# Kernel tuning notes

Measured on AMD Instinct MI355X. Metric: run time of the kernel, lower is better.

The kernel has to match this reference:

```python
import jax, jax.numpy as jnp
import numpy as np

B, S = 32, 4096          # decode batch, kv cache length
HID, H = 5120, 16        # hidden size, local heads
DN, DR, DV = 128, 64, 128  # qk_nope, qk_rope, v head dims
QL, KL = 1536, 512       # q_lora_rank, kv_lora_rank
BASE = 10000.0
EPS = 1e-6
SCALE = (DN + DR) ** -0.5


def rmsnorm(x, w):
    return x * jax.lax.rsqrt(jnp.mean(x * x, axis=-1, keepdims=True) + EPS) * w


def rope_interleaved(x, pos):
    # non-neox (interleaved pairs) rope, per-row positions pos: [B]
    d = x.shape[-1]
    inv = 1.0 / (BASE ** (jnp.arange(0, d, 2, dtype=jnp.float32) / d))  # [d/2]
    fr = pos.astype(jnp.float32)[:, None] * inv                          # [B, d/2]
    cos, sin = jnp.cos(fr), jnp.sin(fr)
    x1, x2 = x[..., 0::2], x[..., 1::2]
    while cos.ndim < x1.ndim:  # broadcast over head dim if present
        cos, sin = cos[:, None], sin[:, None]
    o1 = x1 * cos - x2 * sin
    o2 = x2 * cos + x1 * sin
    return jnp.stack([o1, o2], axis=-1).reshape(x.shape)


def setup_inputs() -> dict:
    key = jax.random.key(0)
    ks = jax.random.split(key, 9)
    w = 0.02  # weight scale for sane activations
    return {
        "hidden_states": jax.random.normal(ks[0], (B, HID), jnp.float32),
        "positions": jax.random.randint(ks[1], (B,), 0, S, jnp.int32),
        "kv_cache_latent": jax.random.normal(ks[2], (B, S, KL), jnp.float32),
        "kv_cache_rope": jax.random.normal(ks[3], (B, S, DR), jnp.float32),
        "w_qkv_a": jax.random.normal(ks[4], (HID, QL + KL + DR), jnp.float32) * w,
        "q_a_norm_w": jnp.ones((QL,), jnp.float32),
        "w_q_b": jax.random.normal(ks[5], (QL, H * (DN + DR)), jnp.float32) * w,
        "kv_a_norm_w": jnp.ones((KL,), jnp.float32),
        "w_kc": jax.random.normal(ks[6], (H, DN, KL), jnp.float32) * w,
        "w_vc": jax.random.normal(ks[7], (H, KL, DV), jnp.float32) * w,
        "w_o": jax.random.normal(ks[8], (H * DV, HID), jnp.float32) * w,
    }


def reference(hidden_states, positions, kv_cache_latent, kv_cache_rope,
              w_qkv_a, q_a_norm_w, w_q_b, kv_a_norm_w, w_kc, w_vc, w_o):
    # fused qkv_a projection -> q_lora | kv latent | k_pe
    qkv = hidden_states @ w_qkv_a                       # [B, QL+KL+DR]
    q_a, latent, k_pe = jnp.split(qkv, [QL, QL + KL], axis=-1)

    # q path: rmsnorm -> q_b_proj -> per-head split nope/pe
    q = (rmsnorm(q_a, q_a_norm_w) @ w_q_b).reshape(B, H, DN + DR)
    q_nope, q_pe = q[..., :DN], q[..., DN:]
    q_pe = rope_interleaved(q_pe, positions)            # [B, H, DR]

    # kv latent path: rmsnorm latent, rope k_pe, write current token into cache
    latent_n = rmsnorm(latent, kv_a_norm_w)             # [B, KL]
    k_pe = rope_interleaved(k_pe, positions)            # [B, DR]
    cache_l = kv_cache_latent.at[:, -1, :].set(latent_n)  # [B, S, KL]
    cache_r = kv_cache_rope.at[:, -1, :].set(k_pe)        # [B, S, DR]

    # weight absorption: q_nope absorbed through w_kc into latent space
    q_abs = jnp.einsum("bhd,hdc->bhc", q_nope, w_kc)    # [B, H, KL]

    # MQA attention over latent KV (1 kv head shared by all q heads)
    scores = (jnp.einsum("bhc,bsc->bhs", q_abs, cache_l)
              + jnp.einsum("bhr,bsr->bhs", q_pe, cache_r)) * SCALE
    attn = jax.nn.softmax(scores, axis=-1)              # [B, H, S]
    ctx = jnp.einsum("bhs,bsc->bhc", attn, cache_l)     # [B, H, KL]

    # un-absorb values through w_vc, then output projection
    out = jnp.einsum("bhc,hcv->bhv", ctx, w_vc).reshape(B, H * DV)
    return out @ w_o                                    # [B, HID]
```

## Files before the change

kernel.cpp:

```cpp
#include <hip/hip_runtime.h>
#include <stdint.h>

#define B_   32
#define S_   4096
#define HID_ 5120
#define H_   16
#define DN_  128
#define DR_  64
#define DV_  128
#define QL_  1536
#define KL_  512
#define KC_  576
#define NQKV_ 2112
#define NQB_  3072
#define EPS_ 1e-6f
#define SCALE_ 0.07216878364870323f

typedef __attribute__((ext_vector_type(4))) float f32x4;
typedef __attribute__((ext_vector_type(8))) short s16x8;
typedef __attribute__((ext_vector_type(4))) unsigned short u16x4;

__device__ __forceinline__ unsigned short f2bf(float f) {
  union { float f; unsigned u; } v; v.f = f;
  unsigned r = v.u + 0x7fffu + ((v.u >> 16) & 1u);
  return (unsigned short)(r >> 16);
}

__global__ void cvt_bf(const float* __restrict__ X, unsigned short* __restrict__ Y, int n4) {
  int i = blockIdx.x * 256 + threadIdx.x;
  if (i < n4) {
    float4 v = ((const float4*)X)[i];
    u16x4 o; o.x = f2bf(v.x); o.y = f2bf(v.y); o.z = f2bf(v.z); o.w = f2bf(v.w);
    ((u16x4*)Y)[i] = o;
  }
}

template<int K, int TK, int N>
__global__ __launch_bounds__(256) void gemm_bf(const unsigned short* __restrict__ Abf,
                                               const float* __restrict__ W,
                                               float* __restrict__ P) {
  int t = threadIdx.x, wave = t >> 6, lane = t & 63;
  int quad = lane >> 4, lo = lane & 15;
  int n0 = blockIdx.x * 64 + wave * 16;
  int k0 = blockIdx.y * TK;
  f32x4 acc0 = {0.f, 0.f, 0.f, 0.f}, acc1 = {0.f, 0.f, 0.f, 0.f};
  const float* wp = W + (size_t)(k0 + quad * 8) * N + n0 + lo;
  const unsigned short* a0p = Abf + (size_t)lo * K + k0 + quad * 8;
  const unsigned short* a1p = Abf + (size_t)(16 + lo) * K + k0 + quad * 8;
#pragma unroll 2
  for (int kk = 0; kk < TK / 32; ++kk) {
    s16x8 a0 = *(const s16x8*)(a0p + kk * 32);
    s16x8 a1 = *(const s16x8*)(a1p + kk * 32);
    float wv[8];
#pragma unroll
    for (int j = 0; j < 8; ++j) wv[j] = wp[((size_t)kk * 32 + j) * N];
    s16x8 bf;
#pragma unroll
    for (int j = 0; j < 8; ++j) bf[j] = (short)f2bf(wv[j]);
    acc0 = __builtin_amdgcn_mfma_f32_16x16x32_bf16(a0, bf, acc0, 0, 0, 0);
    acc1 = __builtin_amdgcn_mfma_f32_16x16x32_bf16(a1, bf, acc1, 0, 0, 0);
  }
  float* p = P + ((size_t)blockIdx.y * B_) * N + n0 + lo;
#pragma unroll
  for (int reg = 0; reg < 4; ++reg) {
    p[(size_t)(quad * 4 + reg) * N]      = acc0[reg];
    p[(size_t)(16 + quad * 4 + reg) * N] = acc1[reg];
  }
}

__global__ void k2a(const float* __restrict__ P1, const float* __restrict__ qw,
                    const float* __restrict__ kvw, const int* __restrict__ pos,
                    unsigned short* __restrict__ qn_bf, float* __restrict__ latent_n,
                    float* __restrict__ kpe_rot, float* __restrict__ cs_buf) {
  int b = blockIdx.x, t = threadIdx.x;
  __shared__ float row[NQKV_];
  __shared__ float red[256], red2[256];
  float sq = 0.f, sl = 0.f;
  for (int n = t; n < NQKV_; n += 256) {
    float s = 0.f;
#pragma unroll
    for (int ks = 0; ks < 16; ++ks) s += P1[((size_t)ks * B_ + b) * NQKV_ + n];
    row[n] = s;
    if (n < QL_) sq += s * s;
    else if (n < QL_ + KL_) sl += s * s;
  }
  red[t] = sq; red2[t] = sl;
  __syncthreads();
  for (int off = 128; off > 0; off >>= 1) {
    if (t < off) { red[t] += red[t + off]; red2[t] += red2[t + off]; }
    __syncthreads();
  }
  float rq = 1.0f / sqrtf(red[0]  / QL_ + EPS_);
  float rl = 1.0f / sqrtf(red2[0] / KL_ + EPS_);
  for (int n = t; n < QL_; n += 256) qn_bf[(size_t)b * QL_ + n] = f2bf(row[n] * rq * qw[n]);
  for (int n = t; n < KL_; n += 256) latent_n[(size_t)b * KL_ + n] = row[QL_ + n] * rl * kvw[n];
  if (t < 32) {
    double inv = exp(-((double)t / 32.0) * log(10000.0));
    float fr = (float)pos[b] * (float)inv;
    float c = (float)cos((double)fr), s = (float)sin((double)fr);
    cs_buf[(b * 32 + t) * 2] = c; cs_buf[(b * 32 + t) * 2 + 1] = s;
    float x1 = row[QL_ + KL_ + 2 * t], x2 = row[QL_ + KL_ + 2 * t + 1];
    kpe_rot[b * DR_ + 2 * t]     = x1 * c - x2 * s;
    kpe_rot[b * DR_ + 2 * t + 1] = x2 * c + x1 * s;
  }
}

__global__ __launch_bounds__(256) void k2c(const float* __restrict__ P2,
                                           const float* __restrict__ w_kc,
                                           const float* __restrict__ cs_buf,
                                           unsigned short* __restrict__ q_cat) {
  int b = blockIdx.y, t = threadIdx.x, wave = t >> 6, lane = t & 63;
  int h = blockIdx.x * 4 + wave;
  __shared__ float qh[4][192];
  for (int j = lane; j < 192; j += 64) {
    float s = 0.f;
    int col = h * 192 + j;
#pragma unroll
    for (int ks = 0; ks < 12; ++ks) s += P2[((size_t)ks * B_ + b) * NQB_ + col];
    qh[wave][j] = s;
  }
  __syncthreads();
  if (lane < 32) {
    float c = cs_buf[(b * 32 + lane) * 2], s = cs_buf[(b * 32 + lane) * 2 + 1];
    float x1 = qh[wave][DN_ + 2 * lane], x2 = qh[wave][DN_ + 2 * lane + 1];
    qh[wave][DN_ + 2 * lane]     = x1 * c - x2 * s;
    qh[wave][DN_ + 2 * lane + 1] = x2 * c + x1 * s;
  }
  __syncthreads();
  float acc[8];
#pragma unroll
  for (int i = 0; i < 8; ++i) acc[i] = 0.f;
  const float* wk = w_kc + (size_t)h * DN_ * KL_;
#pragma unroll 2
  for (int d = 0; d < DN_; ++d) {
    float qd = qh[wave][d];
#pragma unroll
    for (int i = 0; i < 8; ++i)
      acc[i] = fmaf(qd, wk[(size_t)d * KL_ + lane + 64 * i], acc[i]);
  }
  unsigned short* qc = q_cat + ((size_t)b * H_ + h) * KC_;
#pragma unroll
  for (int i = 0; i < 8; ++i) qc[lane + 64 * i] = f2bf(acc[i] * SCALE_);
  qc[KL_ + lane] = f2bf(qh[wave][DN_ + lane] * SCALE_);
}

#define LP_ 584
#define CHUNK_ 256
#define TR_ 32
#define NTL_ 8

__global__ __launch_bounds__(256, 2) void attn(
    const float* __restrict__ cache_l, const float* __restrict__ cache_r,
    const float* __restrict__ latent_n, const float* __restrict__ kpe_rot,
    const unsigned short* __restrict__ q_cat,
    float* __restrict__ ws_acc, float* __restrict__ ws_ml) {
  int chunk = blockIdx.x, b = blockIdx.y;
  int t = threadIdx.x, wave = t >> 6, lane = t & 63;
  int quad = lane >> 4, lo = lane & 15;

  __shared__ __attribute__((aligned(16))) unsigned short Lt[TR_ * LP_];
  __shared__ __attribute__((aligned(16))) unsigned short pb[4][H_ * TR_];

  s16x8 af[18];
  const unsigned short* qc = q_cat + ((size_t)b * H_ + lo) * KC_;
#pragma unroll
  for (int ks = 0; ks < 18; ++ks) af[ks] = *(const s16x8*)(qc + ks * 32 + quad * 8);

  f32x4 accc[NTL_];
#pragma unroll
  for (int i = 0; i < NTL_; ++i) accc[i] = (f32x4){0.f, 0.f, 0.f, 0.f};
  float m_run[4], l_run[4];
#pragma unroll
  for (int r = 0; r < 4; ++r) { m_run[r] = -3.0e38f; l_run[r] = 0.f; }

  int r8 = t >> 3, u = t & 7;

  float4 v[18];
  auto load_tile = [&](int tile) {
    int s = chunk * CHUNK_ + tile * TR_ + r8;
    const float* rl = cache_l + ((size_t)b * S_ + s) * KL_;
    const float* rr = cache_r + ((size_t)b * S_ + s) * DR_;
    if (s == S_ - 1) { rl = latent_n + (size_t)b * KL_; rr = kpe_rot + (size_t)b * DR_; }
#pragma unroll
    for (int j = 0; j < 18; ++j) {
      int c = u * 4 + j * 32;
      v[j] = *(const float4*)((j < 16) ? (rl + c) : (rr + (c - 512)));
    }
  };
  load_tile(0);

#pragma unroll 1
  for (int tile = 0; tile < NTL_; ++tile) {
    __syncthreads();
#pragma unroll
    for (int j = 0; j < 18; ++j) {
      int c = u * 4 + j * 32;
      u16x4 o; o.x = f2bf(v[j].x); o.y = f2bf(v[j].y); o.z = f2bf(v[j].z); o.w = f2bf(v[j].w);
      *(u16x4*)(&Lt[r8 * LP_ + c]) = o;
    }
    if (tile + 1 < NTL_) load_tile(tile + 1);
    __syncthreads();
    f32x4 sc0 = {0.f, 0.f, 0.f, 0.f}, sc1 = {0.f, 0.f, 0.f, 0.f};
#pragma unroll
    for (int ks = 0; ks < 18; ++ks) {
      s16x8 b0 = *(const s16x8*)(&Lt[lo * LP_ + ks * 32 + quad * 8]);
      s16x8 b1 = *(const s16x8*)(&Lt[(16 + lo) * LP_ + ks * 32 + quad * 8]);
      sc0 = __builtin_amdgcn_mfma_f32_16x16x32_bf16(af[ks], b0, sc0, 0, 0, 0);
      sc1 = __builtin_amdgcn_mfma_f32_16x16x32_bf16(af[ks], b1, sc1, 0, 0, 0);
    }
#pragma unroll
    for (int reg = 0; reg < 4; ++reg) {
      float s0 = sc0[reg], s1 = sc1[reg];
      float mt = fmaxf(s0, s1);
#pragma unroll
      for (int m = 1; m < 16; m <<= 1) mt = fmaxf(mt, __shfl_xor(mt, m, 64));
      float mn = fmaxf(m_run[reg], mt);
      float alpha = __expf(m_run[reg] - mn);
      m_run[reg] = mn;
      float p0 = __expf(s0 - mn), p1 = __expf(s1 - mn);
      float lt = p0 + p1;
#pragma unroll
      for (int m = 1; m < 16; m <<= 1) lt += __shfl_xor(lt, m, 64);
      l_run[reg] = l_run[reg] * alpha + lt;
#pragma unroll
      for (int i = 0; i < NTL_; ++i) accc[i][reg] *= alpha;
      int h = quad * 4 + reg;
      pb[wave][h * TR_ + lo]      = f2bf(p0);
      pb[wave][h * TR_ + 16 + lo] = f2bf(p1);
    }
    s16x8 ap = *(const s16x8*)(&pb[wave][lo * TR_ + quad * 8]);
#pragma unroll
    for (int nt = 0; nt < NTL_; ++nt) {
      int c = wave * 128 + nt * 16 + lo;
      s16x8 bv;
#pragma unroll
      for (int j = 0; j < 8; ++j) bv[j] = (short)Lt[(quad * 8 + j) * LP_ + c];
      accc[nt] = __builtin_amdgcn_mfma_f32_16x16x32_bf16(ap, bv, accc[nt], 0, 0, 0);
    }
  }
  float* accp = ws_acc + (((size_t)b * 16 + chunk) * H_) * KL_;
#pragma unroll
  for (int nt = 0; nt < NTL_; ++nt) {
    int c = wave * 128 + nt * 16 + lo;
#pragma unroll
    for (int reg = 0; reg < 4; ++reg)
      accp[(size_t)(quad * 4 + reg) * KL_ + c] = accc[nt][reg];
  }
  if (wave == 0 && lo == 0) {
#pragma unroll
    for (int reg = 0; reg < 4; ++reg) {
      int h = quad * 4 + reg;
      ws_ml[(((size_t)b * 16 + chunk) * H_ + h) * 2 + 0] = m_run[reg];
      ws_ml[(((size_t)b * 16 + chunk) * H_ + h) * 2 + 1] = l_run[reg];
    }
  }
}

__global__ void combine(const float* __restrict__ ws_acc, const float* __restrict__ ws_ml,
                        const float* __restrict__ w_vc, unsigned short* __restrict__ o_v) {
  int h = blockIdx.x, b = blockIdx.y, t = threadIdx.x;
  __shared__ float sm[16], sl[16];
  __shared__ float ctx[KL_];
  __shared__ float ps[256];
  if (t < 16) {
    sm[t] = ws_ml[(((size_t)b * 16 + t) * H_ + h) * 2];
    sl[t] = ws_ml[(((size_t)b * 16 + t) * H_ + h) * 2 + 1];
  }
  __syncthreads();
  float M = -3e38f;
#pragma unroll
  for (int i = 0; i < 16; ++i) M = fmaxf(M, sm[i]);
  float wkk[16]; float Lsum = 0.f;
#pragma unroll
  for (int i = 0; i < 16; ++i) { wkk[i] = __expf(sm[i] - M); Lsum += wkk[i] * sl[i]; }
  float invL = 1.0f / Lsum;
  for (int c = t; c < KL_; c += 256) {
    float s = 0.f;
#pragma unroll
    for (int i = 0; i < 16; ++i)
      s += wkk[i] * ws_acc[(((size_t)b * 16 + i) * H_ + h) * KL_ + c];
    ctx[c] = s * invL;
  }
  __syncthreads();
  int vv = t & 127, half = t >> 7;
  const float* wv = w_vc + (size_t)h * KL_ * DV_;
  float s = 0.f;
#pragma unroll 4
  for (int k = half * 256; k < half * 256 + 256; ++k)
    s = fmaf(ctx[k], wv[(size_t)k * DV_ + vv], s);
  ps[t] = s;
  __syncthreads();
  if (t < 128) o_v[(size_t)b * (H_ * DV_) + h * DV_ + t] = f2bf(ps[t] + ps[t + 128]);
}

__global__ void reduce_out(const float* __restrict__ P, float* __restrict__ out) {
  int i = blockIdx.x * 256 + threadIdx.x;
  float s = 0.f;
#pragma unroll
  for (int ks = 0; ks < 8; ++ks) s += P[(size_t)ks * (B_ * HID_) + i];
  out[i] = s;
}

extern "C" void kernel_launch(void* const* d_in, const int* in_sizes, int n_in,
                              void* d_out, int out_size, void* d_ws, size_t ws_size,
                              hipStream_t stream) {
  const float* hs    = (const float*)d_in[0];
  const int*   pos   = (const int*)d_in[1];
  const float* cl    = (const float*)d_in[2];
  const float* cr    = (const float*)d_in[3];
  const float* w_qkv = (const float*)d_in[4];
  const float* qnw   = (const float*)d_in[5];
  const float* w_qb  = (const float*)d_in[6];
  const float* kvnw  = (const float*)d_in[7];
  const float* w_kc  = (const float*)d_in[8];
  const float* w_vc  = (const float*)d_in[9];
  const float* w_o   = (const float*)d_in[10];
  float* out = (float*)d_out;

  char* ws = (char*)d_ws;
  float* ws_acc = (float*)(ws);
  float* P1     = (float*)(ws + 16777216);
  float* P2     = (float*)(ws + 21102592);
  float* P5     = (float*)(ws + 25821184);
  unsigned short* hs_bf = (unsigned short*)(ws + 31064064);
  unsigned short* qn_bf = (unsigned short*)(ws + 31391744);
  float* latent_n = (float*)(ws + 31490048);
  float* kpe_rot  = (float*)(ws + 31555584);
  float* cs_buf   = (float*)(ws + 31563776);
  unsigned short* q_cat = (unsigned short*)(ws + 31571968);
  float* ws_ml    = (float*)(ws + 32161792);
  unsigned short* o_v_bf = (unsigned short*)(ws + 32227328);

  cvt_bf<<<160, 256, 0, stream>>>(hs, hs_bf, B_ * HID_ / 4);
  gemm_bf<HID_, 320, NQKV_><<<dim3(33, 16), 256, 0, stream>>>(hs_bf, w_qkv, P1);
  k2a<<<32, 256, 0, stream>>>(P1, qnw, kvnw, pos, qn_bf, latent_n, kpe_rot, cs_buf);
  gemm_bf<QL_, 128, NQB_><<<dim3(48, 12), 256, 0, stream>>>(qn_bf, w_qb, P2);
  k2c<<<dim3(4, 32), 256, 0, stream>>>(P2, w_kc, cs_buf, q_cat);
  attn<<<dim3(16, 32), 256, 0, stream>>>(cl, cr, latent_n, kpe_rot, q_cat, ws_acc, ws_ml);
  combine<<<dim3(16, 32), 256, 0, stream>>>(ws_acc, ws_ml, w_vc, o_v_bf);
  gemm_bf<H_ * DV_, 256, HID_><<<dim3(80, 8), 256, 0, stream>>>(o_v_bf, w_o, P5);
  reduce_out<<<640, 256, 0, stream>>>(P5, out);
}
```

Before: 569.4 us.

## Fuse hidden-state bf16 conversion into GEMM and widen split-K across small kernels

Removes the standalone fp32-to-bf16 conversion kernel by converting the hidden states inside a new GEMM variant. Split-K factors are doubled for all three projection GEMMs, and k2a and k2c are split across more blocks. bf16 conversion switches to HIP's packed intrinsics, reduce_out is vectorised, and combine uses two accumulators. The goal is more parallelism for the small GEMMs and fewer launches, at the cost of larger partial-sum buffers and more reduction traffic.

```diff
diff --git a/kernel.cpp b/kernel.cpp
--- a/kernel.cpp
+++ b/kernel.cpp
@@ -1,4 +1,5 @@
 #include <hip/hip_runtime.h>
+#include <hip/hip_bf16.h>
 #include <stdint.h>
 
 #define B_   32
@@ -18,21 +19,23 @@
 
 typedef __attribute__((ext_vector_type(4))) float f32x4;
 typedef __attribute__((ext_vector_type(8))) short s16x8;
-typedef __attribute__((ext_vector_type(4))) unsigned short u16x4;
-
-__device__ __forceinline__ unsigned short f2bf(float f) {
-  union { float f; unsigned u; } v; v.f = f;
-  unsigned r = v.u + 0x7fffu + ((v.u >> 16) & 1u);
-  return (unsigned short)(r >> 16);
-}
-
-__global__ void cvt_bf(const float* __restrict__ X, unsigned short* __restrict__ Y, int n4) {
-  int i = blockIdx.x * 256 + threadIdx.x;
-  if (i < n4) {
-    float4 v = ((const float4*)X)[i];
-    u16x4 o; o.x = f2bf(v.x); o.y = f2bf(v.y); o.z = f2bf(v.z); o.w = f2bf(v.w);
-    ((u16x4*)Y)[i] = o;
-  }
+typedef __attribute__((ext_vector_type(2))) unsigned int u32x2;
+typedef __attribute__((ext_vector_type(4))) unsigned int u32x4;
+
+__device__ __forceinline__ unsigned short bf(float f) {
+  union { __hip_bfloat16 h; unsigned short u; } v;
+  v.h = __float2bfloat16(f);
+  return v.u;
+}
+__device__ __forceinline__ unsigned int bf2(float x, float y) {
+  union { __hip_bfloat162 h; unsigned int u; } v;
+  v.h = __float22bfloat162_rn(float2{x, y});
+  return v.u;
+}
+__device__ __forceinline__ s16x8 pack8(const float* w) {
+  union { u32x4 q; s16x8 s; } v;
+  v.q = (u32x4){bf2(w[0], w[1]), bf2(w[2], w[3]), bf2(w[4], w[5]), bf2(w[6], w[7])};
+  return v.s;
 }
 
 template<int K, int TK, int N>
@@ -54,11 +57,9 @@
     float wv[8];
 #pragma unroll
     for (int j = 0; j < 8; ++j) wv[j] = wp[((size_t)kk * 32 + j) * N];
-    s16x8 bf;
-#pragma unroll
-    for (int j = 0; j < 8; ++j) bf[j] = (short)f2bf(wv[j]);
-    acc0 = __builtin_amdgcn_mfma_f32_16x16x32_bf16(a0, bf, acc0, 0, 0, 0);
-    acc1 = __builtin_amdgcn_mfma_f32_16x16x32_bf16(a1, bf, acc1, 0, 0, 0);
+    s16x8 bfv = pack8(wv);
+    acc0 = __builtin_amdgcn_mfma_f32_16x16x32_bf16(a0, bfv, acc0, 0, 0, 0);
+    acc1 = __builtin_amdgcn_mfma_f32_16x16x32_bf16(a1, bfv, acc1, 0, 0, 0);
   }
   float* p = P + ((size_t)blockIdx.y * B_) * N + n0 + lo;
 #pragma unroll
@@ -68,40 +69,100 @@
   }
 }
 
-__global__ void k2a(const float* __restrict__ P1, const float* __restrict__ qw,
+template<int K, int TK, int N>
+__global__ __launch_bounds__(256) void gemm_f32a(const float* __restrict__ A,
+                                                 const float* __restrict__ W,
+                                                 float* __restrict__ P) {
+  int t = threadIdx.x, wave = t >> 6, lane = t & 63;
+  int quad = lane >> 4, lo = lane & 15;
+  int n0 = blockIdx.x * 64 + wave * 16;
+  int k0 = blockIdx.y * TK;
+  f32x4 acc0 = {0.f, 0.f, 0.f, 0.f}, acc1 = {0.f, 0.f, 0.f, 0.f};
+  const float* wp = W + (size_t)(k0 + quad * 8) * N + n0 + lo;
+  const float* a0p = A + (size_t)lo * K + k0 + quad * 8;
+  const float* a1p = A + (size_t)(16 + lo) * K + k0 + quad * 8;
+#pragma unroll 2
+  for (int kk = 0; kk < TK / 32; ++kk) {
+    f32x4 x0 = *(const f32x4*)(a0p + kk * 32);
+    f32x4 x1 = *(const f32x4*)(a0p + kk * 32 + 4);
+    f32x4 y0 = *(const f32x4*)(a1p + kk * 32);
+    f32x4 y1 = *(const f32x4*)(a1p + kk * 32 + 4);
+    float a0f[8], a1f[8];
+#pragma unroll
+    for (int j = 0; j < 4; ++j) {
+      a0f[j] = x0[j]; a0f[4 + j] = x1[j];
+      a1f[j] = y0[j]; a1f[4 + j] = y1[j];
+    }
+    s16x8 a0 = pack8(a0f);
+    s16x8 a1 = pack8(a1f);
+    float wv[8];
+#pragma unroll
+    for (int j = 0; j < 8; ++j) wv[j] = wp[((size_t)kk * 32 + j) * N];
+    s16x8 bfv = pack8(wv);
+    acc0 = __builtin_amdgcn_mfma_f32_16x16x32_bf16(a0, bfv, acc0, 0, 0, 0);
+    acc1 = __builtin_amdgcn_mfma_f32_16x16x32_bf16(a1, bfv, acc1, 0, 0, 0);
+  }
+  float* p = P + ((size_t)blockIdx.y * B_) * N + n0 + lo;
+#pragma unroll
+  for (int reg = 0; reg < 4; ++reg) {
+    p[(size_t)(quad * 4 + reg) * N]      = acc0[reg];
+    p[(size_t)(16 + quad * 4 + reg) * N] = acc1[reg];
+  }
+}
+
+#define NSL1 32
+#define NSL2 24
+#define NSL3 16
+
+__global__ __launch_bounds__(256) void k2a(const float* __restrict__ P1, const float* __restrict__ qw,
                     const float* __restrict__ kvw, const int* __restrict__ pos,
                     unsigned short* __restrict__ qn_bf, float* __restrict__ latent_n,
                     float* __restrict__ kpe_rot, float* __restrict__ cs_buf) {
-  int b = blockIdx.x, t = threadIdx.x;
-  __shared__ float row[NQKV_];
-  __shared__ float red[256], red2[256];
-  float sq = 0.f, sl = 0.f;
-  for (int n = t; n < NQKV_; n += 256) {
-    float s = 0.f;
-#pragma unroll
-    for (int ks = 0; ks < 16; ++ks) s += P1[((size_t)ks * B_ + b) * NQKV_ + n];
-    row[n] = s;
-    if (n < QL_) sq += s * s;
-    else if (n < QL_ + KL_) sl += s * s;
-  }
-  red[t] = sq; red2[t] = sl;
-  __syncthreads();
-  for (int off = 128; off > 0; off >>= 1) {
-    if (t < off) { red[t] += red[t + off]; red2[t] += red2[t + off]; }
+  int b = blockIdx.y, t = threadIdx.x;
+  __shared__ float row[QL_];
+  __shared__ float red[256];
+  if (blockIdx.x == 0) {
+    float sq = 0.f;
+    for (int n = t; n < QL_; n += 256) {
+      float s = 0.f;
+#pragma unroll
+      for (int ks = 0; ks < NSL1; ++ks) s += P1[((size_t)ks * B_ + b) * NQKV_ + n];
+      row[n] = s; sq += s * s;
+    }
+    red[t] = sq;
     __syncthreads();
-  }
-  float rq = 1.0f / sqrtf(red[0]  / QL_ + EPS_);
-  float rl = 1.0f / sqrtf(red2[0] / KL_ + EPS_);
-  for (int n = t; n < QL_; n += 256) qn_bf[(size_t)b * QL_ + n] = f2bf(row[n] * rq * qw[n]);
-  for (int n = t; n < KL_; n += 256) latent_n[(size_t)b * KL_ + n] = row[QL_ + n] * rl * kvw[n];
-  if (t < 32) {
-    double inv = exp(-((double)t / 32.0) * log(10000.0));
-    float fr = (float)pos[b] * (float)inv;
-    float c = (float)cos((double)fr), s = (float)sin((double)fr);
-    cs_buf[(b * 32 + t) * 2] = c; cs_buf[(b * 32 + t) * 2 + 1] = s;
-    float x1 = row[QL_ + KL_ + 2 * t], x2 = row[QL_ + KL_ + 2 * t + 1];
-    kpe_rot[b * DR_ + 2 * t]     = x1 * c - x2 * s;
-    kpe_rot[b * DR_ + 2 * t + 1] = x2 * c + x1 * s;
+    for (int off = 128; off > 0; off >>= 1) {
+      if (t < off) red[t] += red[t + off];
+      __syncthreads();
+    }
+    float rq = 1.0f / sqrtf(red[0] / QL_ + EPS_);
+    for (int n = t; n < QL_; n += 256) qn_bf[(size_t)b * QL_ + n] = bf(row[n] * rq * qw[n]);
+  } else {
+    float sl = 0.f;
+    for (int n = t; n < KL_ + DR_; n += 256) {
+      float s = 0.f;
+#pragma unroll
+      for (int ks = 0; ks < NSL1; ++ks) s += P1[((size_t)ks * B_ + b) * NQKV_ + QL_ + n];
+      row[n] = s;
+      if (n < KL_) sl += s * s;
+    }
+    red[t] = sl;
+    __syncthreads();
+    for (int off = 128; off > 0; off >>= 1) {
+      if (t < off) red[t] += red[t + off];
+      __syncthreads();
+    }
+    float rl = 1.0f / sqrtf(red[0] / KL_ + EPS_);
+    for (int n = t; n < KL_; n += 256) latent_n[(size_t)b * KL_ + n] = row[n] * rl * kvw[n];
+    if (t < 32) {
+      double inv = exp(-((double)t / 32.0) * log(10000.0));
+      float fr = (float)pos[b] * (float)inv;
+      float c = (float)cos((double)fr), s = (float)sin((double)fr);
+      cs_buf[(b * 32 + t) * 2] = c; cs_buf[(b * 32 + t) * 2 + 1] = s;
+      float x1 = row[KL_ + 2 * t], x2 = row[KL_ + 2 * t + 1];
+      kpe_rot[b * DR_ + 2 * t]     = x1 * c - x2 * s;
+      kpe_rot[b * DR_ + 2 * t + 1] = x2 * c + x1 * s;
+    }
   }
 }
 
@@ -110,38 +171,40 @@
                                            const float* __restrict__ cs_buf,
                                            unsigned short* __restrict__ q_cat) {
   int b = blockIdx.y, t = threadIdx.x, wave = t >> 6, lane = t & 63;
-  int h = blockIdx.x * 4 + wave;
-  __shared__ float qh[4][192];
-  for (int j = lane; j < 192; j += 64) {
+  int hl = blockIdx.x * 2;
+  __shared__ float qh[2][192];
+  for (int j = t; j < 384; j += 256) {
+    int hh = j / 192, jj = j - hh * 192;
     float s = 0.f;
-    int col = h * 192 + j;
-#pragma unroll
-    for (int ks = 0; ks < 12; ++ks) s += P2[((size_t)ks * B_ + b) * NQB_ + col];
-    qh[wave][j] = s;
+    int col = (hl + hh) * 192 + jj;
+#pragma unroll
+    for (int ks = 0; ks < NSL2; ++ks) s += P2[((size_t)ks * B_ + b) * NQB_ + col];
+    qh[hh][jj] = s;
   }
   __syncthreads();
-  if (lane < 32) {
-    float c = cs_buf[(b * 32 + lane) * 2], s = cs_buf[(b * 32 + lane) * 2 + 1];
-    float x1 = qh[wave][DN_ + 2 * lane], x2 = qh[wave][DN_ + 2 * lane + 1];
-    qh[wave][DN_ + 2 * lane]     = x1 * c - x2 * s;
-    qh[wave][DN_ + 2 * lane + 1] = x2 * c + x1 * s;
+  if (t < 64) {
+    int hh = t >> 5, ll = t & 31;
+    float c = cs_buf[(b * 32 + ll) * 2], s = cs_buf[(b * 32 + ll) * 2 + 1];
+    float x1 = qh[hh][DN_ + 2 * ll], x2 = qh[hh][DN_ + 2 * ll + 1];
+    qh[hh][DN_ + 2 * ll]     = x1 * c - x2 * s;
+    qh[hh][DN_ + 2 * ll + 1] = x2 * c + x1 * s;
   }
   __syncthreads();
-  float acc[8];
-#pragma unroll
-  for (int i = 0; i < 8; ++i) acc[i] = 0.f;
-  const float* wk = w_kc + (size_t)h * DN_ * KL_;
+  int hh = wave >> 1, half = wave & 1;
+  int h = hl + hh;
+  float acc[4] = {0.f, 0.f, 0.f, 0.f};
+  const float* wk = w_kc + (size_t)h * DN_ * KL_ + half * 256;
 #pragma unroll 2
   for (int d = 0; d < DN_; ++d) {
-    float qd = qh[wave][d];
-#pragma unroll
-    for (int i = 0; i < 8; ++i)
+    float qd = qh[hh][d];
+#pragma unroll
+    for (int i = 0; i < 4; ++i)
       acc[i] = fmaf(qd, wk[(size_t)d * KL_ + lane + 64 * i], acc[i]);
   }
   unsigned short* qc = q_cat + ((size_t)b * H_ + h) * KC_;
 #pragma unroll
-  for (int i = 0; i < 8; ++i) qc[lane + 64 * i] = f2bf(acc[i] * SCALE_);
-  qc[KL_ + lane] = f2bf(qh[wave][DN_ + lane] * SCALE_);
+  for (int i = 0; i < 4; ++i) qc[half * 256 + lane + 64 * i] = bf(acc[i] * SCALE_);
+  if (half == 0) qc[KL_ + lane] = bf(qh[hh][DN_ + lane] * SCALE_);
 }
 
 #define LP_ 584
@@ -195,8 +258,8 @@
 #pragma unroll
     for (int j = 0; j < 18; ++j) {
       int c = u * 4 + j * 32;
-      u16x4 o; o.x = f2bf(v[j].x); o.y = f2bf(v[j].y); o.z = f2bf(v[j].z); o.w = f2bf(v[j].w);
-      *(u16x4*)(&Lt[r8 * LP_ + c]) = o;
+      u32x2 o; o[0] = bf2(v[j].x, v[j].y); o[1] = bf2(v[j].z, v[j].w);
+      *(u32x2*)(&Lt[r8 * LP_ + c]) = o;
     }
     if (tile + 1 < NTL_) load_tile(tile + 1);
     __syncthreads();
@@ -225,8 +288,8 @@
 #pragma unroll
       for (int i = 0; i < NTL_; ++i) accc[i][reg] *= alpha;
       int h = quad * 4 + reg;
-      pb[wave][h * TR_ + lo]      = f2bf(p0);
-      pb[wave][h * TR_ + 16 + lo] = f2bf(p1);
+      pb[wave][h * TR_ + lo]      = bf(p0);
+      pb[wave][h * TR_ + 16 + lo] = bf(p1);
     }
     s16x8 ap = *(const s16x8*)(&pb[wave][lo * TR_ + quad * 8]);
 #pragma unroll
@@ -256,7 +319,8 @@
   }
 }
 
-__global__ void combine(const float* __restrict__ ws_acc, const float* __restrict__ ws_ml,
+__global__ __launch_bounds__(256) void combine(const float* __restrict__ ws_acc,
+                        const float* __restrict__ ws_ml,
                         const float* __restrict__ w_vc, unsigned short* __restrict__ o_v) {
   int h = blockIdx.x, b = blockIdx.y, t = threadIdx.x;
   __shared__ float sm[16], sl[16];
@@ -284,21 +348,24 @@
   __syncthreads();
   int vv = t & 127, half = t >> 7;
   const float* wv = w_vc + (size_t)h * KL_ * DV_;
-  float s = 0.f;
+  float s0 = 0.f, s1 = 0.f;
 #pragma unroll 4
-  for (int k = half * 256; k < half * 256 + 256; ++k)
-    s = fmaf(ctx[k], wv[(size_t)k * DV_ + vv], s);
-  ps[t] = s;
+  for (int k = half * 256; k < half * 256 + 256; k += 2) {
+    s0 = fmaf(ctx[k],     wv[(size_t)k * DV_ + vv],       s0);
+    s1 = fmaf(ctx[k + 1], wv[(size_t)(k + 1) * DV_ + vv], s1);
+  }
+  ps[t] = s0 + s1;
   __syncthreads();
-  if (t < 128) o_v[(size_t)b * (H_ * DV_) + h * DV_ + t] = f2bf(ps[t] + ps[t + 128]);
-}
-
-__global__ void reduce_out(const float* __restrict__ P, float* __restrict__ out) {
+  if (t < 128) o_v[(size_t)b * (H_ * DV_) + h * DV_ + t] = bf(ps[t] + ps[t + 128]);
+}
+
+__global__ __launch_bounds__(256) void reduce_out(const float* __restrict__ P, float* __restrict__ out) {
   int i = blockIdx.x * 256 + threadIdx.x;
-  float s = 0.f;
-#pragma unroll
-  for (int ks = 0; ks < 8; ++ks) s += P[(size_t)ks * (B_ * HID_) + i];
-  out[i] = s;
+  const f32x4* P4 = (const f32x4*)P;
+  f32x4 s = P4[i];
+#pragma unroll
+  for (int ks = 1; ks < NSL3; ++ks) s += P4[(size_t)ks * 40960 + i];
+  ((f32x4*)out)[i] = s;
 }
 
 extern "C" void kernel_launch(void* const* d_in, const int* in_sizes, int n_in,
@@ -320,24 +387,22 @@
   char* ws = (char*)d_ws;
   float* ws_acc = (float*)(ws);
   float* P1     = (float*)(ws + 16777216);
-  float* P2     = (float*)(ws + 21102592);
-  float* P5     = (float*)(ws + 25821184);
-  unsigned short* hs_bf = (unsigned short*)(ws + 31064064);
-  unsigned short* qn_bf = (unsigned short*)(ws + 31391744);
-  float* latent_n = (float*)(ws + 31490048);
-  float* kpe_rot  = (float*)(ws + 31555584);
-  float* cs_buf   = (float*)(ws + 31563776);
-  unsigned short* q_cat = (unsigned short*)(ws + 31571968);
-  float* ws_ml    = (float*)(ws + 32161792);
-  unsigned short* o_v_bf = (unsigned short*)(ws + 32227328);
-
-  cvt_bf<<<160, 256, 0, stream>>>(hs, hs_bf, B_ * HID_ / 4);
-  gemm_bf<HID_, 320, NQKV_><<<dim3(33, 16), 256, 0, stream>>>(hs_bf, w_qkv, P1);
-  k2a<<<32, 256, 0, stream>>>(P1, qnw, kvnw, pos, qn_bf, latent_n, kpe_rot, cs_buf);
-  gemm_bf<QL_, 128, NQB_><<<dim3(48, 12), 256, 0, stream>>>(qn_bf, w_qb, P2);
-  k2c<<<dim3(4, 32), 256, 0, stream>>>(P2, w_kc, cs_buf, q_cat);
+  float* P2     = (float*)(ws + 25427968);
+  float* P5     = (float*)(ws + 34865152);
+  unsigned short* qn_bf = (unsigned short*)(ws + 45350912);
+  float* latent_n = (float*)(ws + 45449216);
+  float* kpe_rot  = (float*)(ws + 45514752);
+  float* cs_buf   = (float*)(ws + 45522944);
+  unsigned short* q_cat = (unsigned short*)(ws + 45531136);
+  float* ws_ml    = (float*)(ws + 46120960);
+  unsigned short* o_v_bf = (unsigned short*)(ws + 46186496);
+
+  gemm_f32a<HID_, 160, NQKV_><<<dim3(33, 32), 256, 0, stream>>>(hs, w_qkv, P1);
+  k2a<<<dim3(2, 32), 256, 0, stream>>>(P1, qnw, kvnw, pos, qn_bf, latent_n, kpe_rot, cs_buf);
+  gemm_bf<QL_, 64, NQB_><<<dim3(48, 24), 256, 0, stream>>>(qn_bf, w_qb, P2);
+  k2c<<<dim3(8, 32), 256, 0, stream>>>(P2, w_kc, cs_buf, q_cat);
   attn<<<dim3(16, 32), 256, 0, stream>>>(cl, cr, latent_n, kpe_rot, q_cat, ws_acc, ws_ml);
   combine<<<dim3(16, 32), 256, 0, stream>>>(ws_acc, ws_ml, w_vc, o_v_bf);
-  gemm_bf<H_ * DV_, 256, HID_><<<dim3(80, 8), 256, 0, stream>>>(o_v_bf, w_o, P5);
-  reduce_out<<<640, 256, 0, stream>>>(P5, out);
-}
+  gemm_bf<H_ * DV_, 128, HID_><<<dim3(80, 16), 256, 0, stream>>>(o_v_bf, w_o, P5);
+  reduce_out<<<160, 256, 0, stream>>>(P5, out);
+}
```

Measured after the change: 551.3 us. 3.2% less time.
